# Kernel optimization log

Hardware: AMD Instinct MI355X
Metric: run time of the kernel (lower is better)

Reference implementation:

```python
import jax, jax.numpy as jnp
import numpy as np

BETA = 0.02  # soft-argmax temperature (CATs / matchsplat default)


def _resize_bilinear_ac(x, out_h, out_w):
    """Bilinear resize over the last two dims, align_corners=True (matches F.interpolate)."""
    H, W = x.shape[-2], x.shape[-1]
    ys = jnp.linspace(0.0, H - 1.0, out_h)
    xs = jnp.linspace(0.0, W - 1.0, out_w)
    y0 = jnp.floor(ys).astype(jnp.int32)
    y1 = jnp.minimum(y0 + 1, H - 1)
    x0 = jnp.floor(xs).astype(jnp.int32)
    x1 = jnp.minimum(x0 + 1, W - 1)
    wy = (ys - y0).astype(x.dtype)
    wx = (xs - x0).astype(x.dtype)
    rows = x[..., y0, :] * (1.0 - wy)[:, None] + x[..., y1, :] * wy[:, None]
    return rows[..., x0] * (1.0 - wx) + rows[..., x1] * wx


def _correlation(f0, f1):
    # f0, f1: [B, C, H, W] -> dense 4D cost volume [B, H0, W0, H1, W1], scaled by 1/sqrt(C)
    b, c, h, w = f0.shape
    return jnp.einsum('bchw,bcuv->bhwuv', f0, f1) / (c ** 0.5)


def _interpolate4d(x, size):
    # x: [B, ch, h1, w1, h2, w2]; separable bilinear over (h2,w2) then (h1,w1), align_corners=True
    B, ch, h1, w1, h2, w2 = x.shape
    x = _resize_bilinear_ac(x.reshape(B, ch * h1 * w1, h2, w2), size[2], size[3])
    x = x.reshape(B, ch, h1, w1, size[2], size[3])
    x = jnp.transpose(x, (0, 1, 4, 5, 2, 3)).reshape(B, ch * size[2] * size[3], h1, w1)
    x = _resize_bilinear_ac(x, size[0], size[1])
    x = x.reshape(B, ch, size[2], size[3], size[0], size[1])
    return jnp.transpose(x, (0, 1, 4, 5, 2, 3))


def _soft_argmax(corr):
    # corr: [B, Hs*Ws, Ht, Wt]; softmax over source positions per target pixel,
    # then marginal expectations of normalized [-1,1] coordinates.
    b, c, h, w = corr.shape
    prob = jax.nn.softmax(corr / BETA, axis=1).reshape(b, h, w, h, w)
    x_normal = jnp.linspace(-1.0, 1.0, w, dtype=corr.dtype)
    y_normal = jnp.linspace(-1.0, 1.0, h, dtype=corr.dtype)
    grid_x = (prob.sum(axis=1) * x_normal[None, :, None, None]).sum(axis=1)[:, None]  # [B,1,h,w]
    grid_y = (prob.sum(axis=2) * y_normal[None, :, None, None]).sum(axis=1)[:, None]
    return grid_x, grid_y


def _mapping_to_flow(mapping):
    # mapping: [B,2,H,W] normalized coords in [-1,1] -> pixel-space flow (map - identity grid)
    B, _, H, W = mapping.shape
    mx = (mapping[:, 0] + 1.0) * (W - 1) / 2.0
    my = (mapping[:, 1] + 1.0) * (H - 1) / 2.0
    gx = jnp.arange(W, dtype=mapping.dtype)[None, :]
    gy = jnp.arange(H, dtype=mapping.dtype)[:, None]
    return jnp.stack([mx - gx, my - gy], axis=1)


def _forward(feat0_c, feat1_c, feat0_f, feat1_f):
    B = feat0_c.shape[0]
    S = 64
    corr_c = _correlation(feat0_c, feat1_c)                        # [B,32,32,32,32]
    corr_c = _interpolate4d(corr_c[:, None], (S, S, S, S))[:, 0]   # [B,64,64,64,64]
    corr_f = _correlation(feat0_f, feat1_f)                        # [B,64,64,64,64]
    c = ((corr_c + corr_f) * 0.5)[:, None]                         # [B,1,64,64,64,64]
    c_flip = jnp.transpose(c, (0, 1, 4, 5, 2, 3))
    gx, gy = _soft_argmax(c_flip.reshape(B, S * S, S, S))
    flow = _mapping_to_flow(jnp.concatenate([gx, gy], axis=1))
    gxf, gyf = _soft_argmax(c.reshape(B, S * S, S, S))
    flow_flip = _mapping_to_flow(jnp.concatenate([gxf, gyf], axis=1))
    trans_features = jnp.stack([feat0_f, feat1_f], axis=1)         # [B,2,C,64,64]
    tc = jnp.stack([feat0_c, feat1_c], axis=1)
    C = tc.shape[2]
    tc = _resize_bilinear_ac(tc.reshape(B * 2, C, tc.shape[-2], tc.shape[-1]), S, S)
    trans_features_coarse = tc.reshape(B, 2, C, S, S)
    return trans_features, trans_features_coarse, c, c_flip, flow, flow_flip


def setup_inputs():
    key = jax.random.key(0)
    k0, k1, k2, k3 = jax.random.split(key, 4)
    B, C = 2, 128
    return {
        'feat0_c': jax.random.normal(k0, (B, C, 32, 32), dtype=jnp.float32),
        'feat1_c': jax.random.normal(k1, (B, C, 32, 32), dtype=jnp.float32),
        'feat0_f': jax.random.normal(k2, (B, C, 64, 64), dtype=jnp.float32),
        'feat1_f': jax.random.normal(k3, (B, C, 64, 64), dtype=jnp.float32),
    }


def reference(feat0_c, feat1_c, feat0_f, feat1_f):
    return _forward(feat0_c, feat1_c, feat0_f, feat1_f)
```

## Files before the change

kernel.cpp:

```cpp
#include <hip/hip_runtime.h>
#include <math.h>

#define SCALE_C 0.08838834764831845f
#define INV_BETA 50.0f
#define STEP63 (2.0f / 63.0f)

typedef short bf16x8 __attribute__((ext_vector_type(8)));
typedef float f32x4 __attribute__((ext_vector_type(4)));

__device__ __forceinline__ void interp_coef32(int t, int& i0, int& i1, float& w) {
    float s = (float)(t * 31) / 63.0f;
    i0 = (int)floorf(s);
    if (i0 > 31) i0 = 31;
    i1 = i0 + 1;
    if (i1 > 31) i1 = 31;
    w = s - (float)i0;
}

__global__ __launch_bounds__(256) void k_corr_c(const float* __restrict__ f0c,
                                                const float* __restrict__ f1c,
                                                float* __restrict__ ws) {
    __shared__ float As[16][64];
    __shared__ float Bs[16][64];
    const int b = blockIdx.z;
    const int m0 = blockIdx.y * 64, n0 = blockIdx.x * 64;
    const float* A  = f0c + (long long)b * 131072;
    const float* Bp = f1c + (long long)b * 131072;
    const int tid = threadIdx.x;
    const int tx = tid & 15, ty = tid >> 4;
    const int lk = tid >> 4;
    const int lc = (tid & 15) * 4;
    float acc[4][4] = {{0.f}};
    for (int k0 = 0; k0 < 128; k0 += 16) {
        *(float4*)&As[lk][lc] = *(const float4*)&A[(k0 + lk) * 1024 + m0 + lc];
        *(float4*)&Bs[lk][lc] = *(const float4*)&Bp[(k0 + lk) * 1024 + n0 + lc];
        __syncthreads();
#pragma unroll
        for (int kk = 0; kk < 16; ++kk) {
            float4 a4 = *(float4*)&As[kk][ty * 4];
            float4 b4 = *(float4*)&Bs[kk][tx * 4];
            float av[4] = {a4.x, a4.y, a4.z, a4.w};
            float bv[4] = {b4.x, b4.y, b4.z, b4.w};
#pragma unroll
            for (int i = 0; i < 4; ++i)
#pragma unroll
                for (int j = 0; j < 4; ++j)
                    acc[i][j] = fmaf(av[i], bv[j], acc[i][j]);
        }
        __syncthreads();
    }
#pragma unroll
    for (int i = 0; i < 4; ++i) {
        float4 w4 = make_float4(acc[i][0] * SCALE_C, acc[i][1] * SCALE_C,
                                acc[i][2] * SCALE_C, acc[i][3] * SCALE_C);
        *(float4*)&ws[(long long)b * 1048576 + (long long)(m0 + ty * 4 + i) * 1024 + n0 + tx * 4] = w4;
    }
}

__global__ __launch_bounds__(256) void k_split(const float* __restrict__ f0f,
                                               const float* __restrict__ f1f,
                                               unsigned short* __restrict__ hi,
                                               unsigned short* __restrict__ lo) {
    __shared__ unsigned int t[64 * 132];
    const int m = blockIdx.y;
    const int pt = blockIdx.x;
    const float* src = ((m >> 1) ? f1f : f0f) + (size_t)(m & 1) * 524288 + pt * 64;
    const int tid = threadIdx.x;
#pragma unroll
    for (int p = 0; p < 8; ++p) {
        int k = p * 16 + (tid >> 4);
        int px = (tid & 15) * 4;
        float4 v = *(const float4*)&src[(size_t)k * 4096 + px];
        float vv[4] = {v.x, v.y, v.z, v.w};
#pragma unroll
        for (int j = 0; j < 4; ++j) {
            float x = vv[j];
            unsigned int u = __float_as_uint(x);
            unsigned int h = (u + 0x7FFFu + ((u >> 16) & 1u)) >> 16;
            float r = x - __uint_as_float(h << 16);
            unsigned int ur = __float_as_uint(r);
            unsigned int l2 = (ur + 0x7FFFu + ((ur >> 16) & 1u)) >> 16;
            t[(px + j) * 132 + k] = h | (l2 << 16);
        }
    }
    __syncthreads();
    const int row = tid >> 2, ks = (tid & 3) * 32;
    size_t obase = ((size_t)m * 4096 + (size_t)pt * 64 + row) * 128 + ks;
#pragma unroll
    for (int c = 0; c < 4; ++c) {
        unsigned int u[8];
        *(uint4*)&u[0] = *(const uint4*)&t[row * 132 + ks + c * 8];
        *(uint4*)&u[4] = *(const uint4*)&t[row * 132 + ks + c * 8 + 4];
        uint4 ho, lw;
        ho.x = (u[0] & 0xFFFFu) | (u[1] << 16);
        ho.y = (u[2] & 0xFFFFu) | (u[3] << 16);
        ho.z = (u[4] & 0xFFFFu) | (u[5] << 16);
        ho.w = (u[6] & 0xFFFFu) | (u[7] << 16);
        lw.x = (u[0] >> 16) | (u[1] & 0xFFFF0000u);
        lw.y = (u[2] >> 16) | (u[3] & 0xFFFF0000u);
        lw.z = (u[4] >> 16) | (u[5] & 0xFFFF0000u);
        lw.w = (u[6] >> 16) | (u[7] & 0xFFFF0000u);
        *(uint4*)&hi[obase + c * 8] = ho;
        *(uint4*)&lo[obase + c * 8] = lw;
    }
}

__global__ __launch_bounds__(256, 2) void k_fused2(const unsigned short* __restrict__ planes,
                                                   const float* __restrict__ cws,
                                                   float* __restrict__ c_out,
                                                   float* __restrict__ cf_out,
                                                   float* __restrict__ parts) {
    __shared__ __attribute__((aligned(16))) float smem[13440];
    float* const Freg = smem + 9216;
    const int b = blockIdx.z, by = blockIdx.y, bx = blockIdx.x;
    const int tid = threadIdx.x;
    const int wv = tid >> 6, lane = tid & 63;
    const int lr = lane & 15, lq = lane >> 4;
    const int wr = wv >> 1, wc = wv & 1;

    const int y0base = (2 * by * 31) / 63;
    const int y1base = (2 * bx * 31) / 63;

    {
        const float* Cc = cws + (size_t)b * 1048576;
        for (int e = tid; e < 9216; e += 256) {
            int x1c = e & 31;
            int q = e >> 5;
            int r = (q * 21846) >> 16;
            int dy1 = q - r * 3;
            int x0c = r & 31;
            int dy0 = r >> 5;
            int y0r = y0base + dy0; if (y0r > 31) y0r = 31;
            int y1r = y1base + dy1; if (y1r > 31) y1r = 31;
            smem[e] = Cc[(size_t)(y0r * 32 + x0c) * 1024 + y1r * 32 + x1c];
        }
    }
    __syncthreads();

    {
        for (int e = tid; e < 4096; e += 256) {
            int x1c = e & 31, x0c = (e >> 5) & 31, p = e >> 10;
            int s0 = p >> 1, s1 = p & 1;
            int ya, yb; float wy0; interp_coef32(2 * by + s0, ya, yb, wy0);
            int za, zb; float wy1; interp_coef32(2 * bx + s1, za, zb, wy1);
            int a0 = ya - y0base, a1 = yb - y0base;
            int b0 = za - y1base, b1 = zb - y1base;
            const float* s00 = &smem[((a0 * 32 + x0c) * 3) * 32 + x1c];
            const float* s10 = &smem[((a1 * 32 + x0c) * 3) * 32 + x1c];
            float g0 = s00[b0 * 32] * (1.f - wy1) + s00[b1 * 32] * wy1;
            float g1 = s10[b0 * 32] * (1.f - wy1) + s10[b1 * 32] * wy1;
            Freg[(p * 32 + x0c) * 33 + x1c] = g0 * (1.f - wy0) + g1 * wy0;
        }
    }
    __syncthreads();

    {
        for (int e = tid; e < 8192; e += 256) {
            int x1 = e & 63, x0c = (e >> 6) & 31, p = e >> 11;
            int xa, xb; float wx1; interp_coef32(x1, xa, xb, wx1);
            const float* Fp = &Freg[(p * 32 + x0c) * 33];
            smem[(p * 64 + x1) * 33 + x0c] = Fp[xa] * (1.f - wx1) + Fp[xb] * wx1;
        }
    }

    const unsigned short* Ah = planes + (size_t)b * 524288       + (size_t)(by * 128 + wr * 64) * 128;
    const unsigned short* Bh = planes + (size_t)(2 + b) * 524288 + (size_t)(bx * 128 + wc * 64) * 128;
    f32x4 acc[4][4];
#pragma unroll
    for (int i = 0; i < 4; ++i)
#pragma unroll
        for (int j = 0; j < 4; ++j) acc[i][j] = (f32x4){0.f, 0.f, 0.f, 0.f};

#pragma unroll 1
    for (int kc = 0; kc < 4; ++kc) {
        const int ko = kc * 32 + lq * 8;
        bf16x8 ah[4], al[4];
#pragma unroll
        for (int t = 0; t < 4; ++t) {
            const unsigned short* pa = Ah + (size_t)(t * 16 + lr) * 128 + ko;
            ah[t] = *(const bf16x8*)pa;
            al[t] = *(const bf16x8*)(pa + 2097152);
        }
#pragma unroll
        for (int ni = 0; ni < 4; ++ni) {
            const unsigned short* pb = Bh + (size_t)(ni * 16 + lr) * 128 + ko;
            bf16x8 bh = *(const bf16x8*)pb;
            bf16x8 bl = *(const bf16x8*)(pb + 2097152);
#pragma unroll
            for (int mi = 0; mi < 4; ++mi) {
                f32x4 a = acc[mi][ni];
                a = __builtin_amdgcn_mfma_f32_16x16x32_bf16(ah[mi], bh, a, 0, 0, 0);
                a = __builtin_amdgcn_mfma_f32_16x16x32_bf16(al[mi], bh, a, 0, 0, 0);
                a = __builtin_amdgcn_mfma_f32_16x16x32_bf16(ah[mi], bl, a, 0, 0, 0);
                acc[mi][ni] = a;
            }
        }
    }

    __syncthreads();

#pragma unroll
    for (int mi = 0; mi < 4; ++mi)
#pragma unroll
        for (int dr = 0; dr < 4; ++dr) {
            int x0 = mi * 16 + lq * 4 + dr;
            float s = (float)(x0 * 31) / 63.0f;
            int i0 = (int)s;
            float w = s - (float)i0;
            int i1 = i0 + 1; if (i1 > 31) i1 = 31;
#pragma unroll
            for (int ni = 0; ni < 4; ++ni) {
                const float* t2 = &smem[(wv * 64 + ni * 16 + lr) * 33];
                float up = t2[i0] * (1.f - w) + t2[i1] * w;
                acc[mi][ni][dr] = (acc[mi][ni][dr] * SCALE_C + up) * 0.5f;
            }
        }

#pragma unroll
    for (int r = 0; r < 2; ++r) {
        __syncthreads();
        if (wr == r) {
#pragma unroll
            for (int mi = 0; mi < 4; ++mi)
#pragma unroll
                for (int dr = 0; dr < 4; ++dr) {
                    int rl = mi * 16 + lq * 4 + dr;
                    int sw = (rl & 7) << 2;
#pragma unroll
                    for (int ni = 0; ni < 4; ++ni) {
                        int col = wc * 64 + ni * 16 + lr;
                        int c4 = col >> 2;
                        smem[rl * 132 + ((c4 ^ sw) << 2) + (col & 3)] = acc[mi][ni][dr];
                    }
                }
        }
        __syncthreads();
        size_t cb = ((size_t)b << 24) + (size_t)(by * 128 + r * 64) * 4096 + bx * 128;
#pragma unroll
        for (int i = 0; i < 8; ++i) {
            int f = tid + i * 256;
            int rl = f >> 5, c4 = f & 31;
            float4 v = *(float4*)&smem[rl * 132 + ((c4 ^ ((rl & 7) << 2)) << 2)];
            *(float4*)&c_out[cb + (size_t)rl * 4096 + c4 * 4] = v;
        }
    }

#pragma unroll
    for (int r = 0; r < 2; ++r) {
        __syncthreads();
        if (wc == r) {
#pragma unroll
            for (int ni = 0; ni < 4; ++ni) {
                int col = ni * 16 + lr;
                int sw = (col & 7) << 2;
#pragma unroll
                for (int mi = 0; mi < 4; ++mi) {
                    int q = wr * 16 + mi * 4 + lq;
                    *(float4*)&smem[col * 132 + ((q ^ sw) << 2)] =
                        make_float4(acc[mi][ni][0], acc[mi][ni][1], acc[mi][ni][2], acc[mi][ni][3]);
                }
            }
        }
        __syncthreads();
        size_t fb = ((size_t)b << 24) + (size_t)(bx * 128 + r * 64) * 4096 + by * 128;
#pragma unroll
        for (int i = 0; i < 8; ++i) {
            int f = tid + i * 256;
            int col = f >> 5, q = f & 31;
            float4 v = *(float4*)&smem[col * 132 + ((q ^ ((col & 7) << 2)) << 2)];
            *(float4*)&cf_out[fb + (size_t)col * 4096 + q * 4] = v;
        }
    }

    float4* pred4 = (float4*)smem;
    float4* parts4 = (float4*)parts;
    __syncthreads();

    {
        float yn1 = -1.f + (float)(2 * bx + wc) * STEP63;
#pragma unroll
        for (int mi = 0; mi < 4; ++mi)
#pragma unroll
            for (int dr = 0; dr < 4; ++dr) {
                float m = fmaxf(fmaxf(acc[mi][0][dr], acc[mi][1][dr]),
                                fmaxf(acc[mi][2][dr], acc[mi][3][dr]));
                m = fmaxf(m, __shfl_xor(m, 1, 64));
                m = fmaxf(m, __shfl_xor(m, 2, 64));
                m = fmaxf(m, __shfl_xor(m, 4, 64));
                m = fmaxf(m, __shfl_xor(m, 8, 64));
                float l = 0.f, sx = 0.f;
#pragma unroll
                for (int ni = 0; ni < 4; ++ni) {
                    float e = __expf((acc[mi][ni][dr] - m) * INV_BETA);
                    l += e;
                    sx += e * (-1.f + (float)(ni * 16 + lr) * STEP63);
                }
                l += __shfl_xor(l, 1, 64);  sx += __shfl_xor(sx, 1, 64);
                l += __shfl_xor(l, 2, 64);  sx += __shfl_xor(sx, 2, 64);
                l += __shfl_xor(l, 4, 64);  sx += __shfl_xor(sx, 4, 64);
                l += __shfl_xor(l, 8, 64);  sx += __shfl_xor(sx, 8, 64);
                if (lr == 0)
                    pred4[wc * 128 + wr * 64 + mi * 16 + lq * 4 + dr] = make_float4(m, l, sx, yn1 * l);
            }
    }
    __syncthreads();
    if (tid < 128) {
        float4 h0 = pred4[tid], h1 = pred4[128 + tid];
        float M = fmaxf(h0.x, h1.x);
        float s0 = __expf((h0.x - M) * INV_BETA);
        float s1 = __expf((h1.x - M) * INV_BETA);
        parts4[((size_t)b * 4096 + by * 128 + tid) * 32 + bx] =
            make_float4(M, h0.y * s0 + h1.y * s1, h0.z * s0 + h1.z * s1, h0.w * s0 + h1.w * s1);
    }
    __syncthreads();

    {
        float yn0 = -1.f + (float)(2 * by + wr) * STEP63;
#pragma unroll
        for (int ni = 0; ni < 4; ++ni) {
            float m = acc[0][ni][0];
#pragma unroll
            for (int mi = 0; mi < 4; ++mi)
#pragma unroll
                for (int dr = 0; dr < 4; ++dr) m = fmaxf(m, acc[mi][ni][dr]);
            m = fmaxf(m, __shfl_xor(m, 16, 64));
            m = fmaxf(m, __shfl_xor(m, 32, 64));
            float l = 0.f, sx = 0.f;
#pragma unroll
            for (int mi = 0; mi < 4; ++mi)
#pragma unroll
                for (int dr = 0; dr < 4; ++dr) {
                    float e = __expf((acc[mi][ni][dr] - m) * INV_BETA);
                    l += e;
                    sx += e * (-1.f + (float)(mi * 16 + lq * 4 + dr) * STEP63);
                }
            l += __shfl_xor(l, 16, 64);  sx += __shfl_xor(sx, 16, 64);
            l += __shfl_xor(l, 32, 64);  sx += __shfl_xor(sx, 32, 64);
            if (lq == 0)
                pred4[wr * 128 + wc * 64 + ni * 16 + lr] = make_float4(m, l, sx, yn0 * l);
        }
    }
    __syncthreads();
    if (tid < 128) {
        float4 h0 = pred4[tid], h1 = pred4[128 + tid];
        float M = fmaxf(h0.x, h1.x);
        float s0 = __expf((h0.x - M) * INV_BETA);
        float s1 = __expf((h1.x - M) * INV_BETA);
        parts4[262144 + ((size_t)b * 4096 + bx * 128 + tid) * 32 + by] =
            make_float4(M, h0.y * s0 + h1.y * s1, h0.z * s0 + h1.z * s1, h0.w * s0 + h1.w * s1);
    }
}

__global__ __launch_bounds__(256) void k_flow(const float* __restrict__ parts,
                                              float* __restrict__ flow,
                                              float* __restrict__ flowf) {
    const int row = blockIdx.x * 4 + (threadIdx.x >> 6);
    const int lane = threadIdx.x & 63;
    const float4* p4 = (const float4*)parts + (long long)row * 32;
    float m = -1e30f, l = 0.f, sx = 0.f, sy = 0.f;
    if (lane < 32) { float4 v = p4[lane]; m = v.x; l = v.y; sx = v.z; sy = v.w; }
    float M = m;
#pragma unroll
    for (int off = 1; off < 64; off <<= 1) M = fmaxf(M, __shfl_xor(M, off, 64));
    float s = __expf((m - M) * INV_BETA);
    l *= s; sx *= s; sy *= s;
#pragma unroll
    for (int off = 1; off < 64; off <<= 1) {
        l += __shfl_xor(l, off, 64);
        sx += __shfl_xor(sx, off, 64);
        sy += __shfl_xor(sy, off, 64);
    }
    if (lane == 0) {
        float gx = sx / l, gy = sy / l;
        float mx = (gx + 1.f) * 31.5f, my = (gy + 1.f) * 31.5f;
        int dir = row >> 13, b = (row >> 12) & 1, p = row & 4095;
        float* o = dir ? flowf : flow;
        o[(long long)b * 8192 + p] = mx - (float)(p & 63);
        o[(long long)b * 8192 + 4096 + p] = my - (float)(p >> 6);
    }
}

__global__ void k_copy_trans(const float* __restrict__ f0f, const float* __restrict__ f1f,
                             float* __restrict__ out1) {
    int idx = blockIdx.x * 256 + threadIdx.x;
    int bv = idx >> 17;
    int r = idx & 131071;
    int b = bv >> 1, v = bv & 1;
    const float4* src = (const float4*)(v ? f1f : f0f) + (long long)b * 131072 + r;
    ((float4*)out1)[idx] = *src;
}

__global__ void k_coarse(const float* __restrict__ f0c, const float* __restrict__ f1c,
                         float* __restrict__ out2) {
    int idx = blockIdx.x * 256 + threadIdx.x;
    int x = idx & 63, y = (idx >> 6) & 63, ch = (idx >> 12) & 127;
    int v = (idx >> 19) & 1, b = idx >> 20;
    int iy0, iy1; float wy; interp_coef32(y, iy0, iy1, wy);
    int ix0, ix1; float wx; interp_coef32(x, ix0, ix1, wx);
    const float* src = (v ? f1c : f0c) + (long long)(b * 128 + ch) * 1024;
    float a  = src[iy0 * 32 + ix0] * (1.f - wy) + src[iy1 * 32 + ix0] * wy;
    float c2 = src[iy0 * 32 + ix1] * (1.f - wy) + src[iy1 * 32 + ix1] * wy;
    out2[idx] = a * (1.f - wx) + c2 * wx;
}

__global__ __launch_bounds__(256) void k_fused_fb(const float* __restrict__ f0f,
                                                  const float* __restrict__ f1f,
                                                  const float* __restrict__ cws,
                                                  float* __restrict__ c_out,
                                                  float* __restrict__ cf_out) {
    __shared__ float As[16][64];
    __shared__ float Bs[16][64];
    __shared__ float tmp[32][33];
    const int b = blockIdx.z, y0 = blockIdx.y, y1 = blockIdx.x;
    const int tid = threadIdx.x;
    const int tx = tid & 15, ty = tid >> 4;
    const float* A  = f0f + (long long)b * 524288 + y0 * 64;
    const float* Bp = f1f + (long long)b * 524288 + y1 * 64;
    int iy0a, iy0b; float wy0; interp_coef32(y0, iy0a, iy0b, wy0);
    int iy1a, iy1b; float wy1; interp_coef32(y1, iy1a, iy1b, wy1);
    const float* Cc = cws + (long long)b * 1048576;
    for (int r = tid; r < 1024; r += 256) {
        int i = r >> 5, j = r & 31;
        const float* ra = Cc + (long long)(iy0a * 32 + i) * 1024;
        const float* rb = Cc + (long long)(iy0b * 32 + i) * 1024;
        float va = ra[iy1a * 32 + j] * (1.f - wy1) + ra[iy1b * 32 + j] * wy1;
        float vb = rb[iy1a * 32 + j] * (1.f - wy1) + rb[iy1b * 32 + j] * wy1;
        tmp[i][j] = va * (1.f - wy0) + vb * wy0;
    }
    float acc[4][4] = {{0.f}};
    const int lk = tid >> 4;
    const int lc = (tid & 15) * 4;
    for (int k0 = 0; k0 < 128; k0 += 16) {
        *(float4*)&As[lk][lc] = *(const float4*)&A[(long long)(k0 + lk) * 4096 + lc];
        *(float4*)&Bs[lk][lc] = *(const float4*)&Bp[(long long)(k0 + lk) * 4096 + lc];
        __syncthreads();
#pragma unroll
        for (int kk = 0; kk < 16; ++kk) {
            float4 a4 = *(float4*)&As[kk][ty * 4];
            float4 b4 = *(float4*)&Bs[kk][tx * 4];
            float av[4] = {a4.x, a4.y, a4.z, a4.w};
            float bv[4] = {b4.x, b4.y, b4.z, b4.w};
#pragma unroll
            for (int i = 0; i < 4; ++i)
#pragma unroll
                for (int j = 0; j < 4; ++j)
                    acc[i][j] = fmaf(av[i], bv[j], acc[i][j]);
        }
        __syncthreads();
    }
    int ix0a[4], ix0b[4]; float wx0[4];
    int ix1a[4], ix1b[4]; float wx1[4];
#pragma unroll
    for (int i = 0; i < 4; ++i) interp_coef32(ty * 4 + i, ix0a[i], ix0b[i], wx0[i]);
#pragma unroll
    for (int j = 0; j < 4; ++j) interp_coef32(tx * 4 + j, ix1a[j], ix1b[j], wx1[j]);
    float val[4][4];
#pragma unroll
    for (int i = 0; i < 4; ++i)
#pragma unroll
        for (int j = 0; j < 4; ++j) {
            float ta = tmp[ix0a[i]][ix1a[j]] * (1.f - wx1[j]) + tmp[ix0a[i]][ix1b[j]] * wx1[j];
            float tb = tmp[ix0b[i]][ix1a[j]] * (1.f - wx1[j]) + tmp[ix0b[i]][ix1b[j]] * wx1[j];
            val[i][j] = (acc[i][j] * SCALE_C + (ta * (1.f - wx0[i]) + tb * wx0[i])) * 0.5f;
        }
    const long long cbase = ((long long)b << 24) + (long long)(y0 * 64) * 4096 + y1 * 64;
#pragma unroll
    for (int i = 0; i < 4; ++i)
        *(float4*)&c_out[cbase + (long long)(ty * 4 + i) * 4096 + tx * 4] =
            make_float4(val[i][0], val[i][1], val[i][2], val[i][3]);
    const long long fbase = ((long long)b << 24) + (long long)(y1 * 64) * 4096 + y0 * 64;
#pragma unroll
    for (int j = 0; j < 4; ++j)
        *(float4*)&cf_out[fbase + (long long)(tx * 4 + j) * 4096 + ty * 4] =
            make_float4(val[0][j], val[1][j], val[2][j], val[3][j]);
}

__global__ __launch_bounds__(256) void k_softargmax(const float* __restrict__ cmat,
                                                    float* __restrict__ flow_out) {
    const int tid = threadIdx.x;
    const float4* src = (const float4*)cmat + (long long)blockIdx.x * 1024;
    float4 r0 = src[tid];
    float4 r1 = src[tid + 256];
    float4 r2 = src[tid + 512];
    float4 r3 = src[tid + 768];
    float m = fmaxf(fmaxf(fmaxf(r0.x, r0.y), fmaxf(r0.z, r0.w)),
                    fmaxf(fmaxf(r1.x, r1.y), fmaxf(r1.z, r1.w)));
    m = fmaxf(m, fmaxf(fmaxf(r2.x, r2.y), fmaxf(r2.z, r2.w)));
    m = fmaxf(m, fmaxf(fmaxf(r3.x, r3.y), fmaxf(r3.z, r3.w)));
    __shared__ float red[16];
    const int lane = tid & 63, wave = tid >> 6;
#pragma unroll
    for (int off = 32; off > 0; off >>= 1) m = fmaxf(m, __shfl_xor(m, off, 64));
    if (lane == 0) red[wave] = m;
    __syncthreads();
    m = fmaxf(fmaxf(red[0], red[1]), fmaxf(red[2], red[3]));
    float l = 0.f, sx = 0.f, sy = 0.f;
#pragma unroll
    for (int s = 0; s < 4; ++s) {
        float4 r = (s == 0) ? r0 : (s == 1) ? r1 : (s == 2) ? r2 : r3;
        int f = tid + s * 256;
        float yn = -1.f + (float)(f >> 4) * STEP63;
        float xb = (float)((f & 15) * 4);
        float e0 = __expf((r.x - m) * 50.f);
        float e1 = __expf((r.y - m) * 50.f);
        float e2 = __expf((r.z - m) * 50.f);
        float e3 = __expf((r.w - m) * 50.f);
        float es = e0 + e1 + e2 + e3;
        l += es;
        sy += es * yn;
        sx += e0 * (-1.f + xb * STEP63) + e1 * (-1.f + (xb + 1.f) * STEP63)
            + e2 * (-1.f + (xb + 2.f) * STEP63) + e3 * (-1.f + (xb + 3.f) * STEP63);
    }
#pragma unroll
    for (int off = 32; off > 0; off >>= 1) {
        l  += __shfl_xor(l, off, 64);
        sx += __shfl_xor(sx, off, 64);
        sy += __shfl_xor(sy, off, 64);
    }
    if (lane == 0) { red[4 + wave] = l; red[8 + wave] = sx; red[12 + wave] = sy; }
    __syncthreads();
    if (tid == 0) {
        float L  = red[4] + red[5] + red[6] + red[7];
        float SX = red[8] + red[9] + red[10] + red[11];
        float SY = red[12] + red[13] + red[14] + red[15];
        float mx = (SX / L + 1.f) * 31.5f;
        float my = (SY / L + 1.f) * 31.5f;
        int bi = blockIdx.x;
        int b = bi >> 12, p = bi & 4095;
        flow_out[(long long)b * 8192 + p]        = mx - (float)(p & 63);
        flow_out[(long long)b * 8192 + 4096 + p] = my - (float)(p >> 6);
    }
}

extern "C" void kernel_launch(void* const* d_in, const int* in_sizes, int n_in,
                              void* d_out, int out_size, void* d_ws, size_t ws_size,
                              hipStream_t stream) {
    const float* f0c = (const float*)d_in[0];
    const float* f1c = (const float*)d_in[1];
    const float* f0f = (const float*)d_in[2];
    const float* f1f = (const float*)d_in[3];
    float* out = (float*)d_out;

    float* c_out  = out + 4194304;
    float* cf_out = out + 37748736;
    float* flow   = out + 71303168;
    float* flowf  = out + 71319552;

    if (ws_size >= (size_t)16777216) {
        float* parts = (float*)d_ws;
        float* cws   = parts + 2097152;
        unsigned short* hi = (unsigned short*)out;
        unsigned short* lo = hi + 2097152;
        k_split<<<dim3(64, 4, 1), 256, 0, stream>>>(f0f, f1f, hi, lo);
        k_corr_c<<<dim3(16, 16, 2), 256, 0, stream>>>(f0c, f1c, cws);
        k_fused2<<<dim3(32, 32, 2), 256, 0, stream>>>(hi, cws, c_out, cf_out, parts);
        k_flow<<<4096, 256, 0, stream>>>(parts, flow, flowf);
        k_copy_trans<<<2048, 256, 0, stream>>>(f0f, f1f, out);
        k_coarse<<<8192, 256, 0, stream>>>(f0c, f1c, out + 2097152);
    } else {
        float* corr_ws = out;
        k_corr_c<<<dim3(16, 16, 2), 256, 0, stream>>>(f0c, f1c, corr_ws);
        k_fused_fb<<<dim3(64, 64, 2), 256, 0, stream>>>(f0f, f1f, corr_ws, c_out, cf_out);
        k_copy_trans<<<2048, 256, 0, stream>>>(f0f, f1f, out);
        k_coarse<<<8192, 256, 0, stream>>>(f0c, f1c, out + 2097152);
        k_softargmax<<<8192, 256, 0, stream>>>(c_out, flow);
        k_softargmax<<<8192, 256, 0, stream>>>(cf_out, flowf);
    }
}
```

Baseline: 408.0 us.

## Merge head and tail launches; compute coarse upsample directly from global in fused kernel

Merges k_split and k_corr_c into one k_head launch, and k_flow, k_copy_trans and k_coarse into one k_tail launch, with blocks branching on blockIdx, so fewer kernels are launched. In k_fused2, the staged shared-memory gather and two-pass upsampling of the coarse correlation are replaced by a single pass that reads the eight bilinear taps straight from global memory. This cuts shared memory from about 52KB to 33KB and raises the occupancy hint from 2 to 3 blocks per CU. The trade-off is more global and L2 reads of the coarse volume, plus more register pressure under the tighter launch bound.

```diff
diff --git a/kernel.cpp b/kernel.cpp
--- a/kernel.cpp
+++ b/kernel.cpp
@@ -15,6 +15,369 @@
     i1 = i0 + 1;
     if (i1 > 31) i1 = 31;
     w = s - (float)i0;
+}
+
+__global__ __launch_bounds__(256) void k_head(const float* __restrict__ f0f,
+                                              const float* __restrict__ f1f,
+                                              unsigned short* __restrict__ hi,
+                                              unsigned short* __restrict__ lo,
+                                              const float* __restrict__ f0c,
+                                              const float* __restrict__ f1c,
+                                              float* __restrict__ cws) {
+    __shared__ unsigned int t[64 * 132];
+    __shared__ float As[16][64];
+    __shared__ float Bs[16][64];
+    const int tid = threadIdx.x;
+    if (blockIdx.x < 256) {
+        const int m = blockIdx.x >> 6;
+        const int pt = blockIdx.x & 63;
+        const float* src = ((m >> 1) ? f1f : f0f) + (size_t)(m & 1) * 524288 + pt * 64;
+#pragma unroll
+        for (int p = 0; p < 8; ++p) {
+            int k = p * 16 + (tid >> 4);
+            int px = (tid & 15) * 4;
+            float4 v = *(const float4*)&src[(size_t)k * 4096 + px];
+            float vv[4] = {v.x, v.y, v.z, v.w};
+#pragma unroll
+            for (int j = 0; j < 4; ++j) {
+                float x = vv[j];
+                unsigned int u = __float_as_uint(x);
+                unsigned int h = (u + 0x7FFFu + ((u >> 16) & 1u)) >> 16;
+                float r = x - __uint_as_float(h << 16);
+                unsigned int ur = __float_as_uint(r);
+                unsigned int l2 = (ur + 0x7FFFu + ((ur >> 16) & 1u)) >> 16;
+                t[(px + j) * 132 + k] = h | (l2 << 16);
+            }
+        }
+        __syncthreads();
+        const int row = tid >> 2, ks = (tid & 3) * 32;
+        size_t obase = ((size_t)m * 4096 + (size_t)pt * 64 + row) * 128 + ks;
+#pragma unroll
+        for (int c = 0; c < 4; ++c) {
+            unsigned int u[8];
+            *(uint4*)&u[0] = *(const uint4*)&t[row * 132 + ks + c * 8];
+            *(uint4*)&u[4] = *(const uint4*)&t[row * 132 + ks + c * 8 + 4];
+            uint4 ho, lw;
+            ho.x = (u[0] & 0xFFFFu) | (u[1] << 16);
+            ho.y = (u[2] & 0xFFFFu) | (u[3] << 16);
+            ho.z = (u[4] & 0xFFFFu) | (u[5] << 16);
+            ho.w = (u[6] & 0xFFFFu) | (u[7] << 16);
+            lw.x = (u[0] >> 16) | (u[1] & 0xFFFF0000u);
+            lw.y = (u[2] >> 16) | (u[3] & 0xFFFF0000u);
+            lw.z = (u[4] >> 16) | (u[5] & 0xFFFF0000u);
+            lw.w = (u[6] >> 16) | (u[7] & 0xFFFF0000u);
+            *(uint4*)&hi[obase + c * 8] = ho;
+            *(uint4*)&lo[obase + c * 8] = lw;
+        }
+    } else {
+        const int cid = blockIdx.x - 256;
+        const int b = cid >> 8;
+        const int m0 = ((cid >> 4) & 15) * 64, n0 = (cid & 15) * 64;
+        const float* A  = f0c + (long long)b * 131072;
+        const float* Bp = f1c + (long long)b * 131072;
+        const int tx = tid & 15, ty = tid >> 4;
+        const int lk = tid >> 4;
+        const int lc = (tid & 15) * 4;
+        float acc[4][4] = {{0.f}};
+        for (int k0 = 0; k0 < 128; k0 += 16) {
+            *(float4*)&As[lk][lc] = *(const float4*)&A[(k0 + lk) * 1024 + m0 + lc];
+            *(float4*)&Bs[lk][lc] = *(const float4*)&Bp[(k0 + lk) * 1024 + n0 + lc];
+            __syncthreads();
+#pragma unroll
+            for (int kk = 0; kk < 16; ++kk) {
+                float4 a4 = *(float4*)&As[kk][ty * 4];
+                float4 b4 = *(float4*)&Bs[kk][tx * 4];
+                float av[4] = {a4.x, a4.y, a4.z, a4.w};
+                float bv[4] = {b4.x, b4.y, b4.z, b4.w};
+#pragma unroll
+                for (int i = 0; i < 4; ++i)
+#pragma unroll
+                    for (int j = 0; j < 4; ++j)
+                        acc[i][j] = fmaf(av[i], bv[j], acc[i][j]);
+            }
+            __syncthreads();
+        }
+#pragma unroll
+        for (int i = 0; i < 4; ++i) {
+            float4 w4 = make_float4(acc[i][0] * SCALE_C, acc[i][1] * SCALE_C,
+                                    acc[i][2] * SCALE_C, acc[i][3] * SCALE_C);
+            *(float4*)&cws[(long long)b * 1048576 + (long long)(m0 + ty * 4 + i) * 1024 + n0 + tx * 4] = w4;
+        }
+    }
+}
+
+__global__ __launch_bounds__(256, 3) void k_fused2(const unsigned short* __restrict__ planes,
+                                                   const float* __restrict__ cws,
+                                                   float* __restrict__ c_out,
+                                                   float* __restrict__ cf_out,
+                                                   float* __restrict__ parts) {
+    __shared__ __attribute__((aligned(16))) float smem[8448];
+    const int b = blockIdx.z, by = blockIdx.y, bx = blockIdx.x;
+    const int tid = threadIdx.x;
+    const int wv = tid >> 6, lane = tid & 63;
+    const int lr = lane & 15, lq = lane >> 4;
+    const int wr = wv >> 1, wc = wv & 1;
+
+    {
+        const float* Cc = cws + (size_t)b * 1048576;
+        for (int e = tid; e < 8192; e += 256) {
+            int x1 = e & 63, x0c = (e >> 6) & 31, p = e >> 11;
+            int s0 = p >> 1, s1 = p & 1;
+            int ya, yb; float wy0; interp_coef32(2 * by + s0, ya, yb, wy0);
+            int za, zb; float wy1; interp_coef32(2 * bx + s1, za, zb, wy1);
+            int xa, xb; float wx1; interp_coef32(x1, xa, xb, wx1);
+            const float* r0 = Cc + (size_t)(ya * 32 + x0c) * 1024;
+            const float* r1 = Cc + (size_t)(yb * 32 + x0c) * 1024;
+            float g0 = (r0[za * 32 + xa] * (1.f - wy1) + r0[zb * 32 + xa] * wy1) * (1.f - wy0)
+                     + (r1[za * 32 + xa] * (1.f - wy1) + r1[zb * 32 + xa] * wy1) * wy0;
+            float g1 = (r0[za * 32 + xb] * (1.f - wy1) + r0[zb * 32 + xb] * wy1) * (1.f - wy0)
+                     + (r1[za * 32 + xb] * (1.f - wy1) + r1[zb * 32 + xb] * wy1) * wy0;
+            smem[(p * 64 + x1) * 33 + x0c] = g0 * (1.f - wx1) + g1 * wx1;
+        }
+    }
+
+    const unsigned short* Ah = planes + (size_t)b * 524288       + (size_t)(by * 128 + wr * 64) * 128;
+    const unsigned short* Bh = planes + (size_t)(2 + b) * 524288 + (size_t)(bx * 128 + wc * 64) * 128;
+    f32x4 acc[4][4];
+#pragma unroll
+    for (int i = 0; i < 4; ++i)
+#pragma unroll
+        for (int j = 0; j < 4; ++j) acc[i][j] = (f32x4){0.f, 0.f, 0.f, 0.f};
+
+#pragma unroll 1
+    for (int kc = 0; kc < 4; ++kc) {
+        const int ko = kc * 32 + lq * 8;
+        bf16x8 ah[4], al[4];
+#pragma unroll
+        for (int t = 0; t < 4; ++t) {
+            const unsigned short* pa = Ah + (size_t)(t * 16 + lr) * 128 + ko;
+            ah[t] = *(const bf16x8*)pa;
+            al[t] = *(const bf16x8*)(pa + 2097152);
+        }
+#pragma unroll
+        for (int ni = 0; ni < 4; ++ni) {
+            const unsigned short* pb = Bh + (size_t)(ni * 16 + lr) * 128 + ko;
+            bf16x8 bh = *(const bf16x8*)pb;
+            bf16x8 bl = *(const bf16x8*)(pb + 2097152);
+#pragma unroll
+            for (int mi = 0; mi < 4; ++mi) {
+                f32x4 a = acc[mi][ni];
+                a = __builtin_amdgcn_mfma_f32_16x16x32_bf16(ah[mi], bh, a, 0, 0, 0);
+                a = __builtin_amdgcn_mfma_f32_16x16x32_bf16(al[mi], bh, a, 0, 0, 0);
+                a = __builtin_amdgcn_mfma_f32_16x16x32_bf16(ah[mi], bl, a, 0, 0, 0);
+                acc[mi][ni] = a;
+            }
+        }
+    }
+
+    __syncthreads();
+
+#pragma unroll
+    for (int mi = 0; mi < 4; ++mi)
+#pragma unroll
+        for (int dr = 0; dr < 4; ++dr) {
+            int x0 = mi * 16 + lq * 4 + dr;
+            float s = (float)(x0 * 31) / 63.0f;
+            int i0 = (int)s;
+            float w = s - (float)i0;
+            int i1 = i0 + 1; if (i1 > 31) i1 = 31;
+#pragma unroll
+            for (int ni = 0; ni < 4; ++ni) {
+                const float* t2 = &smem[(wv * 64 + ni * 16 + lr) * 33];
+                float up = t2[i0] * (1.f - w) + t2[i1] * w;
+                acc[mi][ni][dr] = (acc[mi][ni][dr] * SCALE_C + up) * 0.5f;
+            }
+        }
+
+#pragma unroll
+    for (int r = 0; r < 2; ++r) {
+        __syncthreads();
+        if (wr == r) {
+#pragma unroll
+            for (int mi = 0; mi < 4; ++mi)
+#pragma unroll
+                for (int dr = 0; dr < 4; ++dr) {
+                    int rl = mi * 16 + lq * 4 + dr;
+                    int sw = (rl & 7) << 2;
+#pragma unroll
+                    for (int ni = 0; ni < 4; ++ni) {
+                        int col = wc * 64 + ni * 16 + lr;
+                        int c4 = col >> 2;
+                        smem[rl * 132 + ((c4 ^ sw) << 2) + (col & 3)] = acc[mi][ni][dr];
+                    }
+                }
+        }
+        __syncthreads();
+        size_t cb = ((size_t)b << 24) + (size_t)(by * 128 + r * 64) * 4096 + bx * 128;
+#pragma unroll
+        for (int i = 0; i < 8; ++i) {
+            int f = tid + i * 256;
+            int rl = f >> 5, c4 = f & 31;
+            float4 v = *(float4*)&smem[rl * 132 + ((c4 ^ ((rl & 7) << 2)) << 2)];
+            *(float4*)&c_out[cb + (size_t)rl * 4096 + c4 * 4] = v;
+        }
+    }
+
+#pragma unroll
+    for (int r = 0; r < 2; ++r) {
+        __syncthreads();
+        if (wc == r) {
+#pragma unroll
+            for (int ni = 0; ni < 4; ++ni) {
+                int col = ni * 16 + lr;
+                int sw = (col & 7) << 2;
+#pragma unroll
+                for (int mi = 0; mi < 4; ++mi) {
+                    int q = wr * 16 + mi * 4 + lq;
+                    *(float4*)&smem[col * 132 + ((q ^ sw) << 2)] =
+                        make_float4(acc[mi][ni][0], acc[mi][ni][1], acc[mi][ni][2], acc[mi][ni][3]);
+                }
+            }
+        }
+        __syncthreads();
+        size_t fb = ((size_t)b << 24) + (size_t)(bx * 128 + r * 64) * 4096 + by * 128;
+#pragma unroll
+        for (int i = 0; i < 8; ++i) {
+            int f = tid + i * 256;
+            int col = f >> 5, q = f & 31;
+            float4 v = *(float4*)&smem[col * 132 + ((q ^ ((col & 7) << 2)) << 2)];
+            *(float4*)&cf_out[fb + (size_t)col * 4096 + q * 4] = v;
+        }
+    }
+
+    float4* pred4 = (float4*)smem;
+    float4* parts4 = (float4*)parts;
+    __syncthreads();
+
+    {
+        float yn1 = -1.f + (float)(2 * bx + wc) * STEP63;
+#pragma unroll
+        for (int mi = 0; mi < 4; ++mi)
+#pragma unroll
+            for (int dr = 0; dr < 4; ++dr) {
+                float m = fmaxf(fmaxf(acc[mi][0][dr], acc[mi][1][dr]),
+                                fmaxf(acc[mi][2][dr], acc[mi][3][dr]));
+                m = fmaxf(m, __shfl_xor(m, 1, 64));
+                m = fmaxf(m, __shfl_xor(m, 2, 64));
+                m = fmaxf(m, __shfl_xor(m, 4, 64));
+                m = fmaxf(m, __shfl_xor(m, 8, 64));
+                float l = 0.f, sx = 0.f;
+#pragma unroll
+                for (int ni = 0; ni < 4; ++ni) {
+                    float e = __expf((acc[mi][ni][dr] - m) * INV_BETA);
+                    l += e;
+                    sx += e * (-1.f + (float)(ni * 16 + lr) * STEP63);
+                }
+                l += __shfl_xor(l, 1, 64);  sx += __shfl_xor(sx, 1, 64);
+                l += __shfl_xor(l, 2, 64);  sx += __shfl_xor(sx, 2, 64);
+                l += __shfl_xor(l, 4, 64);  sx += __shfl_xor(sx, 4, 64);
+                l += __shfl_xor(l, 8, 64);  sx += __shfl_xor(sx, 8, 64);
+                if (lr == 0)
+                    pred4[wc * 128 + wr * 64 + mi * 16 + lq * 4 + dr] = make_float4(m, l, sx, yn1 * l);
+            }
+    }
+    __syncthreads();
+    if (tid < 128) {
+        float4 h0 = pred4[tid], h1 = pred4[128 + tid];
+        float M = fmaxf(h0.x, h1.x);
+        float s0 = __expf((h0.x - M) * INV_BETA);
+        float s1 = __expf((h1.x - M) * INV_BETA);
+        parts4[((size_t)b * 4096 + by * 128 + tid) * 32 + bx] =
+            make_float4(M, h0.y * s0 + h1.y * s1, h0.z * s0 + h1.z * s1, h0.w * s0 + h1.w * s1);
+    }
+    __syncthreads();
+
+    {
+        float yn0 = -1.f + (float)(2 * by + wr) * STEP63;
+#pragma unroll
+        for (int ni = 0; ni < 4; ++ni) {
+            float m = acc[0][ni][0];
+#pragma unroll
+            for (int mi = 0; mi < 4; ++mi)
+#pragma unroll
+                for (int dr = 0; dr < 4; ++dr) m = fmaxf(m, acc[mi][ni][dr]);
+            m = fmaxf(m, __shfl_xor(m, 16, 64));
+            m = fmaxf(m, __shfl_xor(m, 32, 64));
+            float l = 0.f, sx = 0.f;
+#pragma unroll
+            for (int mi = 0; mi < 4; ++mi)
+#pragma unroll
+                for (int dr = 0; dr < 4; ++dr) {
+                    float e = __expf((acc[mi][ni][dr] - m) * INV_BETA);
+                    l += e;
+                    sx += e * (-1.f + (float)(mi * 16 + lq * 4 + dr) * STEP63);
+                }
+            l += __shfl_xor(l, 16, 64);  sx += __shfl_xor(sx, 16, 64);
+            l += __shfl_xor(l, 32, 64);  sx += __shfl_xor(sx, 32, 64);
+            if (lq == 0)
+                pred4[wr * 128 + wc * 64 + ni * 16 + lr] = make_float4(m, l, sx, yn0 * l);
+        }
+    }
+    __syncthreads();
+    if (tid < 128) {
+        float4 h0 = pred4[tid], h1 = pred4[128 + tid];
+        float M = fmaxf(h0.x, h1.x);
+        float s0 = __expf((h0.x - M) * INV_BETA);
+        float s1 = __expf((h1.x - M) * INV_BETA);
+        parts4[262144 + ((size_t)b * 4096 + bx * 128 + tid) * 32 + by] =
+            make_float4(M, h0.y * s0 + h1.y * s1, h0.z * s0 + h1.z * s1, h0.w * s0 + h1.w * s1);
+    }
+}
+
+__global__ __launch_bounds__(256) void k_tail(const float* __restrict__ parts,
+                                              float* __restrict__ flow,
+                                              float* __restrict__ flowf,
+                                              const float* __restrict__ f0f,
+                                              const float* __restrict__ f1f,
+                                              float* __restrict__ out1,
+                                              const float* __restrict__ f0c,
+                                              const float* __restrict__ f1c,
+                                              float* __restrict__ out2) {
+    const int bid = blockIdx.x;
+    const int tid = threadIdx.x;
+    if (bid < 4096) {
+        const int row = bid * 4 + (tid >> 6);
+        const int lane = tid & 63;
+        const float4* p4 = (const float4*)parts + (long long)row * 32;
+        float m = -1e30f, l = 0.f, sx = 0.f, sy = 0.f;
+        if (lane < 32) { float4 v = p4[lane]; m = v.x; l = v.y; sx = v.z; sy = v.w; }
+        float M = m;
+#pragma unroll
+        for (int off = 1; off < 64; off <<= 1) M = fmaxf(M, __shfl_xor(M, off, 64));
+        float s = __expf((m - M) * INV_BETA);
+        l *= s; sx *= s; sy *= s;
+#pragma unroll
+        for (int off = 1; off < 64; off <<= 1) {
+            l += __shfl_xor(l, off, 64);
+            sx += __shfl_xor(sx, off, 64);
+            sy += __shfl_xor(sy, off, 64);
+        }
+        if (lane == 0) {
+            float gx = sx / l, gy = sy / l;
+            float mx = (gx + 1.f) * 31.5f, my = (gy + 1.f) * 31.5f;
+            int dir = row >> 13, b = (row >> 12) & 1, p = row & 4095;
+            float* o = dir ? flowf : flow;
+            o[(long long)b * 8192 + p] = mx - (float)(p & 63);
+            o[(long long)b * 8192 + 4096 + p] = my - (float)(p >> 6);
+        }
+    } else if (bid < 6144) {
+        int idx = (bid - 4096) * 256 + tid;
+        int bv = idx >> 17;
+        int r = idx & 131071;
+        int b = bv >> 1, v = bv & 1;
+        const float4* src = (const float4*)(v ? f1f : f0f) + (long long)b * 131072 + r;
+        ((float4*)out1)[idx] = *src;
+    } else {
+        int idx = (bid - 6144) * 256 + tid;
+        int x = idx & 63, y = (idx >> 6) & 63, ch = (idx >> 12) & 127;
+        int v = (idx >> 19) & 1, b = idx >> 20;
+        int iy0, iy1; float wy; interp_coef32(y, iy0, iy1, wy);
+        int ix0, ix1; float wx; interp_coef32(x, ix0, ix1, wx);
+        const float* src = (v ? f1c : f0c) + (long long)(b * 128 + ch) * 1024;
+        float a  = src[iy0 * 32 + ix0] * (1.f - wy) + src[iy1 * 32 + ix0] * wy;
+        float c2 = src[iy0 * 32 + ix1] * (1.f - wy) + src[iy1 * 32 + ix1] * wy;
+        out2[idx] = a * (1.f - wx) + c2 * wx;
+    }
 }
 
 __global__ __launch_bounds__(256) void k_corr_c(const float* __restrict__ f0c,
@@ -54,329 +417,6 @@
         float4 w4 = make_float4(acc[i][0] * SCALE_C, acc[i][1] * SCALE_C,
                                 acc[i][2] * SCALE_C, acc[i][3] * SCALE_C);
         *(float4*)&ws[(long long)b * 1048576 + (long long)(m0 + ty * 4 + i) * 1024 + n0 + tx * 4] = w4;
-    }
-}
-
-__global__ __launch_bounds__(256) void k_split(const float* __restrict__ f0f,
-                                               const float* __restrict__ f1f,
-                                               unsigned short* __restrict__ hi,
-                                               unsigned short* __restrict__ lo) {
-    __shared__ unsigned int t[64 * 132];
-    const int m = blockIdx.y;
-    const int pt = blockIdx.x;
-    const float* src = ((m >> 1) ? f1f : f0f) + (size_t)(m & 1) * 524288 + pt * 64;
-    const int tid = threadIdx.x;
-#pragma unroll
-    for (int p = 0; p < 8; ++p) {
-        int k = p * 16 + (tid >> 4);
-        int px = (tid & 15) * 4;
-        float4 v = *(const float4*)&src[(size_t)k * 4096 + px];
-        float vv[4] = {v.x, v.y, v.z, v.w};
-#pragma unroll
-        for (int j = 0; j < 4; ++j) {
-            float x = vv[j];
-            unsigned int u = __float_as_uint(x);
-            unsigned int h = (u + 0x7FFFu + ((u >> 16) & 1u)) >> 16;
-            float r = x - __uint_as_float(h << 16);
-            unsigned int ur = __float_as_uint(r);
-            unsigned int l2 = (ur + 0x7FFFu + ((ur >> 16) & 1u)) >> 16;
-            t[(px + j) * 132 + k] = h | (l2 << 16);
-        }
-    }
-    __syncthreads();
-    const int row = tid >> 2, ks = (tid & 3) * 32;
-    size_t obase = ((size_t)m * 4096 + (size_t)pt * 64 + row) * 128 + ks;
-#pragma unroll
-    for (int c = 0; c < 4; ++c) {
-        unsigned int u[8];
-        *(uint4*)&u[0] = *(const uint4*)&t[row * 132 + ks + c * 8];
-        *(uint4*)&u[4] = *(const uint4*)&t[row * 132 + ks + c * 8 + 4];
-        uint4 ho, lw;
-        ho.x = (u[0] & 0xFFFFu) | (u[1] << 16);
-        ho.y = (u[2] & 0xFFFFu) | (u[3] << 16);
-        ho.z = (u[4] & 0xFFFFu) | (u[5] << 16);
-        ho.w = (u[6] & 0xFFFFu) | (u[7] << 16);
-        lw.x = (u[0] >> 16) | (u[1] & 0xFFFF0000u);
-        lw.y = (u[2] >> 16) | (u[3] & 0xFFFF0000u);
-        lw.z = (u[4] >> 16) | (u[5] & 0xFFFF0000u);
-        lw.w = (u[6] >> 16) | (u[7] & 0xFFFF0000u);
-        *(uint4*)&hi[obase + c * 8] = ho;
-        *(uint4*)&lo[obase + c * 8] = lw;
-    }
-}
-
-__global__ __launch_bounds__(256, 2) void k_fused2(const unsigned short* __restrict__ planes,
-                                                   const float* __restrict__ cws,
-                                                   float* __restrict__ c_out,
-                                                   float* __restrict__ cf_out,
-                                                   float* __restrict__ parts) {
-    __shared__ __attribute__((aligned(16))) float smem[13440];
-    float* const Freg = smem + 9216;
-    const int b = blockIdx.z, by = blockIdx.y, bx = blockIdx.x;
-    const int tid = threadIdx.x;
-    const int wv = tid >> 6, lane = tid & 63;
-    const int lr = lane & 15, lq = lane >> 4;
-    const int wr = wv >> 1, wc = wv & 1;
-
-    const int y0base = (2 * by * 31) / 63;
-    const int y1base = (2 * bx * 31) / 63;
-
-    {
-        const float* Cc = cws + (size_t)b * 1048576;
-        for (int e = tid; e < 9216; e += 256) {
-            int x1c = e & 31;
-            int q = e >> 5;
-            int r = (q * 21846) >> 16;
-            int dy1 = q - r * 3;
-            int x0c = r & 31;
-            int dy0 = r >> 5;
-            int y0r = y0base + dy0; if (y0r > 31) y0r = 31;
-            int y1r = y1base + dy1; if (y1r > 31) y1r = 31;
-            smem[e] = Cc[(size_t)(y0r * 32 + x0c) * 1024 + y1r * 32 + x1c];
-        }
-    }
-    __syncthreads();
-
-    {
-        for (int e = tid; e < 4096; e += 256) {
-            int x1c = e & 31, x0c = (e >> 5) & 31, p = e >> 10;
-            int s0 = p >> 1, s1 = p & 1;
-            int ya, yb; float wy0; interp_coef32(2 * by + s0, ya, yb, wy0);
-            int za, zb; float wy1; interp_coef32(2 * bx + s1, za, zb, wy1);
-            int a0 = ya - y0base, a1 = yb - y0base;
-            int b0 = za - y1base, b1 = zb - y1base;
-            const float* s00 = &smem[((a0 * 32 + x0c) * 3) * 32 + x1c];
-            const float* s10 = &smem[((a1 * 32 + x0c) * 3) * 32 + x1c];
-            float g0 = s00[b0 * 32] * (1.f - wy1) + s00[b1 * 32] * wy1;
-            float g1 = s10[b0 * 32] * (1.f - wy1) + s10[b1 * 32] * wy1;
-            Freg[(p * 32 + x0c) * 33 + x1c] = g0 * (1.f - wy0) + g1 * wy0;
-        }
-    }
-    __syncthreads();
-
-    {
-        for (int e = tid; e < 8192; e += 256) {
-            int x1 = e & 63, x0c = (e >> 6) & 31, p = e >> 11;
-            int xa, xb; float wx1; interp_coef32(x1, xa, xb, wx1);
-            const float* Fp = &Freg[(p * 32 + x0c) * 33];
-            smem[(p * 64 + x1) * 33 + x0c] = Fp[xa] * (1.f - wx1) + Fp[xb] * wx1;
-        }
-    }
-
-    const unsigned short* Ah = planes + (size_t)b * 524288       + (size_t)(by * 128 + wr * 64) * 128;
-    const unsigned short* Bh = planes + (size_t)(2 + b) * 524288 + (size_t)(bx * 128 + wc * 64) * 128;
-    f32x4 acc[4][4];
-#pragma unroll
-    for (int i = 0; i < 4; ++i)
-#pragma unroll
-        for (int j = 0; j < 4; ++j) acc[i][j] = (f32x4){0.f, 0.f, 0.f, 0.f};
-
-#pragma unroll 1
-    for (int kc = 0; kc < 4; ++kc) {
-        const int ko = kc * 32 + lq * 8;
-        bf16x8 ah[4], al[4];
-#pragma unroll
-        for (int t = 0; t < 4; ++t) {
-            const unsigned short* pa = Ah + (size_t)(t * 16 + lr) * 128 + ko;
-            ah[t] = *(const bf16x8*)pa;
-            al[t] = *(const bf16x8*)(pa + 2097152);
-        }
-#pragma unroll
-        for (int ni = 0; ni < 4; ++ni) {
-            const unsigned short* pb = Bh + (size_t)(ni * 16 + lr) * 128 + ko;
-            bf16x8 bh = *(const bf16x8*)pb;
-            bf16x8 bl = *(const bf16x8*)(pb + 2097152);
-#pragma unroll
-            for (int mi = 0; mi < 4; ++mi) {
-                f32x4 a = acc[mi][ni];
-                a = __builtin_amdgcn_mfma_f32_16x16x32_bf16(ah[mi], bh, a, 0, 0, 0);
-                a = __builtin_amdgcn_mfma_f32_16x16x32_bf16(al[mi], bh, a, 0, 0, 0);
-                a = __builtin_amdgcn_mfma_f32_16x16x32_bf16(ah[mi], bl, a, 0, 0, 0);
-                acc[mi][ni] = a;
-            }
-        }
-    }
-
-    __syncthreads();
-
-#pragma unroll
-    for (int mi = 0; mi < 4; ++mi)
-#pragma unroll
-        for (int dr = 0; dr < 4; ++dr) {
-            int x0 = mi * 16 + lq * 4 + dr;
-            float s = (float)(x0 * 31) / 63.0f;
-            int i0 = (int)s;
-            float w = s - (float)i0;
-            int i1 = i0 + 1; if (i1 > 31) i1 = 31;
-#pragma unroll
-            for (int ni = 0; ni < 4; ++ni) {
-                const float* t2 = &smem[(wv * 64 + ni * 16 + lr) * 33];
-                float up = t2[i0] * (1.f - w) + t2[i1] * w;
-                acc[mi][ni][dr] = (acc[mi][ni][dr] * SCALE_C + up) * 0.5f;
-            }
-        }
-
-#pragma unroll
-    for (int r = 0; r < 2; ++r) {
-        __syncthreads();
-        if (wr == r) {
-#pragma unroll
-            for (int mi = 0; mi < 4; ++mi)
-#pragma unroll
-                for (int dr = 0; dr < 4; ++dr) {
-                    int rl = mi * 16 + lq * 4 + dr;
-                    int sw = (rl & 7) << 2;
-#pragma unroll
-                    for (int ni = 0; ni < 4; ++ni) {
-                        int col = wc * 64 + ni * 16 + lr;
-                        int c4 = col >> 2;
-                        smem[rl * 132 + ((c4 ^ sw) << 2) + (col & 3)] = acc[mi][ni][dr];
-                    }
-                }
-        }
-        __syncthreads();
-        size_t cb = ((size_t)b << 24) + (size_t)(by * 128 + r * 64) * 4096 + bx * 128;
-#pragma unroll
-        for (int i = 0; i < 8; ++i) {
-            int f = tid + i * 256;
-            int rl = f >> 5, c4 = f & 31;
-            float4 v = *(float4*)&smem[rl * 132 + ((c4 ^ ((rl & 7) << 2)) << 2)];
-            *(float4*)&c_out[cb + (size_t)rl * 4096 + c4 * 4] = v;
-        }
-    }
-
-#pragma unroll
-    for (int r = 0; r < 2; ++r) {
-        __syncthreads();
-        if (wc == r) {
-#pragma unroll
-            for (int ni = 0; ni < 4; ++ni) {
-                int col = ni * 16 + lr;
-                int sw = (col & 7) << 2;
-#pragma unroll
-                for (int mi = 0; mi < 4; ++mi) {
-                    int q = wr * 16 + mi * 4 + lq;
-                    *(float4*)&smem[col * 132 + ((q ^ sw) << 2)] =
-                        make_float4(acc[mi][ni][0], acc[mi][ni][1], acc[mi][ni][2], acc[mi][ni][3]);
-                }
-            }
-        }
-        __syncthreads();
-        size_t fb = ((size_t)b << 24) + (size_t)(bx * 128 + r * 64) * 4096 + by * 128;
-#pragma unroll
-        for (int i = 0; i < 8; ++i) {
-            int f = tid + i * 256;
-            int col = f >> 5, q = f & 31;
-            float4 v = *(float4*)&smem[col * 132 + ((q ^ ((col & 7) << 2)) << 2)];
-            *(float4*)&cf_out[fb + (size_t)col * 4096 + q * 4] = v;
-        }
-    }
-
-    float4* pred4 = (float4*)smem;
-    float4* parts4 = (float4*)parts;
-    __syncthreads();
-
-    {
-        float yn1 = -1.f + (float)(2 * bx + wc) * STEP63;
-#pragma unroll
-        for (int mi = 0; mi < 4; ++mi)
-#pragma unroll
-            for (int dr = 0; dr < 4; ++dr) {
-                float m = fmaxf(fmaxf(acc[mi][0][dr], acc[mi][1][dr]),
-                                fmaxf(acc[mi][2][dr], acc[mi][3][dr]));
-                m = fmaxf(m, __shfl_xor(m, 1, 64));
-                m = fmaxf(m, __shfl_xor(m, 2, 64));
-                m = fmaxf(m, __shfl_xor(m, 4, 64));
-                m = fmaxf(m, __shfl_xor(m, 8, 64));
-                float l = 0.f, sx = 0.f;
-#pragma unroll
-                for (int ni = 0; ni < 4; ++ni) {
-                    float e = __expf((acc[mi][ni][dr] - m) * INV_BETA);
-                    l += e;
-                    sx += e * (-1.f + (float)(ni * 16 + lr) * STEP63);
-                }
-                l += __shfl_xor(l, 1, 64);  sx += __shfl_xor(sx, 1, 64);
-                l += __shfl_xor(l, 2, 64);  sx += __shfl_xor(sx, 2, 64);
-                l += __shfl_xor(l, 4, 64);  sx += __shfl_xor(sx, 4, 64);
-                l += __shfl_xor(l, 8, 64);  sx += __shfl_xor(sx, 8, 64);
-                if (lr == 0)
-                    pred4[wc * 128 + wr * 64 + mi * 16 + lq * 4 + dr] = make_float4(m, l, sx, yn1 * l);
-            }
-    }
-    __syncthreads();
-    if (tid < 128) {
-        float4 h0 = pred4[tid], h1 = pred4[128 + tid];
-        float M = fmaxf(h0.x, h1.x);
-        float s0 = __expf((h0.x - M) * INV_BETA);
-        float s1 = __expf((h1.x - M) * INV_BETA);
-        parts4[((size_t)b * 4096 + by * 128 + tid) * 32 + bx] =
-            make_float4(M, h0.y * s0 + h1.y * s1, h0.z * s0 + h1.z * s1, h0.w * s0 + h1.w * s1);
-    }
-    __syncthreads();
-
-    {
-        float yn0 = -1.f + (float)(2 * by + wr) * STEP63;
-#pragma unroll
-        for (int ni = 0; ni < 4; ++ni) {
-            float m = acc[0][ni][0];
-#pragma unroll
-            for (int mi = 0; mi < 4; ++mi)
-#pragma unroll
-                for (int dr = 0; dr < 4; ++dr) m = fmaxf(m, acc[mi][ni][dr]);
-            m = fmaxf(m, __shfl_xor(m, 16, 64));
-            m = fmaxf(m, __shfl_xor(m, 32, 64));
-            float l = 0.f, sx = 0.f;
-#pragma unroll
-            for (int mi = 0; mi < 4; ++mi)
-#pragma unroll
-                for (int dr = 0; dr < 4; ++dr) {
-                    float e = __expf((acc[mi][ni][dr] - m) * INV_BETA);
-                    l += e;
-                    sx += e * (-1.f + (float)(mi * 16 + lq * 4 + dr) * STEP63);
-                }
-            l += __shfl_xor(l, 16, 64);  sx += __shfl_xor(sx, 16, 64);
-            l += __shfl_xor(l, 32, 64);  sx += __shfl_xor(sx, 32, 64);
-            if (lq == 0)
-                pred4[wr * 128 + wc * 64 + ni * 16 + lr] = make_float4(m, l, sx, yn0 * l);
-        }
-    }
-    __syncthreads();
-    if (tid < 128) {
-        float4 h0 = pred4[tid], h1 = pred4[128 + tid];
-        float M = fmaxf(h0.x, h1.x);
-        float s0 = __expf((h0.x - M) * INV_BETA);
-        float s1 = __expf((h1.x - M) * INV_BETA);
-        parts4[262144 + ((size_t)b * 4096 + bx * 128 + tid) * 32 + by] =
-            make_float4(M, h0.y * s0 + h1.y * s1, h0.z * s0 + h1.z * s1, h0.w * s0 + h1.w * s1);
-    }
-}
-
-__global__ __launch_bounds__(256) void k_flow(const float* __restrict__ parts,
-                                              float* __restrict__ flow,
-                                              float* __restrict__ flowf) {
-    const int row = blockIdx.x * 4 + (threadIdx.x >> 6);
-    const int lane = threadIdx.x & 63;
-    const float4* p4 = (const float4*)parts + (long long)row * 32;
-    float m = -1e30f, l = 0.f, sx = 0.f, sy = 0.f;
-    if (lane < 32) { float4 v = p4[lane]; m = v.x; l = v.y; sx = v.z; sy = v.w; }
-    float M = m;
-#pragma unroll
-    for (int off = 1; off < 64; off <<= 1) M = fmaxf(M, __shfl_xor(M, off, 64));
-    float s = __expf((m - M) * INV_BETA);
-    l *= s; sx *= s; sy *= s;
-#pragma unroll
-    for (int off = 1; off < 64; off <<= 1) {
-        l += __shfl_xor(l, off, 64);
-        sx += __shfl_xor(sx, off, 64);
-        sy += __shfl_xor(sy, off, 64);
-    }
-    if (lane == 0) {
-        float gx = sx / l, gy = sy / l;
-        float mx = (gx + 1.f) * 31.5f, my = (gy + 1.f) * 31.5f;
-        int dir = row >> 13, b = (row >> 12) & 1, p = row & 4095;
-        float* o = dir ? flowf : flow;
-        o[(long long)b * 8192 + p] = mx - (float)(p & 63);
-        o[(long long)b * 8192 + 4096 + p] = my - (float)(p >> 6);
     }
 }
 
@@ -551,12 +591,9 @@
         float* cws   = parts + 2097152;
         unsigned short* hi = (unsigned short*)out;
         unsigned short* lo = hi + 2097152;
-        k_split<<<dim3(64, 4, 1), 256, 0, stream>>>(f0f, f1f, hi, lo);
-        k_corr_c<<<dim3(16, 16, 2), 256, 0, stream>>>(f0c, f1c, cws);
+        k_head<<<768, 256, 0, stream>>>(f0f, f1f, hi, lo, f0c, f1c, cws);
         k_fused2<<<dim3(32, 32, 2), 256, 0, stream>>>(hi, cws, c_out, cf_out, parts);
-        k_flow<<<4096, 256, 0, stream>>>(parts, flow, flowf);
-        k_copy_trans<<<2048, 256, 0, stream>>>(f0f, f1f, out);
-        k_coarse<<<8192, 256, 0, stream>>>(f0c, f1c, out + 2097152);
+        k_tail<<<14336, 256, 0, stream>>>(parts, flow, flowf, f0f, f1f, out, f0c, f1c, out + 2097152);
     } else {
         float* corr_ws = out;
         k_corr_c<<<dim3(16, 16, 2), 256, 0, stream>>>(f0c, f1c, corr_ws);
```

After: 399.3 us. 2.1% less time.
